# Kernel tuning notes

Hardware: AMD Instinct MI355X
Metric: run time of the kernel (lower is better)

The kernel has to match this reference:

```python
import jax, jax.numpy as jnp
import numpy as np

VOCAB = 32000
HIDDEN = 512
B, T = 8, 512
LN_EPS = 1e-5


def setup_inputs() -> dict:
    key = jax.random.key(0)
    ks = jax.random.split(key, 9)
    s = 0.02
    return {
        "input_ids": jax.random.randint(ks[0], (B, T), 0, VOCAB),
        "emb": jax.random.normal(ks[1], (VOCAB, HIDDEN), jnp.float32) * s,
        "w_ih": jax.random.normal(ks[2], (3 * HIDDEN, HIDDEN), jnp.float32) * s,
        "w_hh": jax.random.normal(ks[3], (3 * HIDDEN, HIDDEN), jnp.float32) * s,
        "b_ih": jnp.zeros((3 * HIDDEN,), jnp.float32),
        "b_hh": jnp.zeros((3 * HIDDEN,), jnp.float32),
        "ln_gamma": jnp.ones((HIDDEN,), jnp.float32),
        "ln_beta": jnp.zeros((HIDDEN,), jnp.float32),
        "head_w": jax.random.normal(ks[4], (VOCAB, HIDDEN), jnp.float32) * s,
        "head_b": jnp.zeros((VOCAB,), jnp.float32),
    }


def _gru_scan(xg, w_hh, b_hh):
    # xg: [T, B, 3H]  (input-side gate pre-activations, PyTorch gate order r,z,n)
    H = xg.shape[-1] // 3
    h0 = jnp.zeros((xg.shape[1], H), xg.dtype)

    def step(h, xg_t):
        hg = h @ w_hh.T + b_hh              # [B, 3H]
        xr, xz, xn = jnp.split(xg_t, 3, axis=-1)
        hr, hz, hn = jnp.split(hg, 3, axis=-1)
        r = jax.nn.sigmoid(xr + hr)
        z = jax.nn.sigmoid(xz + hz)
        n = jnp.tanh(xn + r * hn)
        h_new = (1.0 - z) * n + z * h
        return h_new, h_new

    _, hs = jax.lax.scan(step, h0, xg)
    return hs  # [T, B, H]


def reference(input_ids, emb, w_ih, w_hh, b_ih, b_hh, ln_gamma, ln_beta, head_w, head_b):
    # embedding lookup: [B, T, H]
    x = emb[input_ids]
    # precompute input-side gate pre-activations for all timesteps: [B, T, 3H]
    xg = jnp.einsum("bth,gh->btg", x, w_ih) + b_ih
    # sequential GRU over time
    hs = _gru_scan(jnp.swapaxes(xg, 0, 1), w_hh, b_hh)  # [T, B, H]
    hs = jnp.swapaxes(hs, 0, 1)                          # [B, T, H]
    # LayerNorm over hidden dim
    mu = jnp.mean(hs, axis=-1, keepdims=True)
    var = jnp.mean(jnp.square(hs - mu), axis=-1, keepdims=True)
    y = (hs - mu) * jax.lax.rsqrt(var + LN_EPS) * ln_gamma + ln_beta
    # output head: [B, T, V]
    logits = jnp.einsum("bth,vh->btv", y, head_w) + head_b
    return logits
```

## Files before the change

### kernel.cpp

```cpp
#include <hip/hip_runtime.h>
#include <hip/hip_bf16.h>
#include <stdint.h>

#define VOCAB 32000
#define HID 512
#define NB 8
#define SEQ 512
#define NG 1536
#define LN_EPS 1e-5f
#define GRU_WGS 32
#define GRU_SPIN_BUDGET (1 << 20)

typedef short bf16x8 __attribute__((ext_vector_type(8)));
typedef float f32x4 __attribute__((ext_vector_type(4)));

__device__ __forceinline__ unsigned short f2bf(float f) {
  union { float f; uint32_t u; } c; c.f = f;
  return (unsigned short)((c.u + 0x7fffu + ((c.u >> 16) & 1u)) >> 16);
}

__global__ void init_ws_kernel(unsigned short* h_state, int* flags) {
  int i = blockIdx.x * 256 + threadIdx.x;
  if (i < 2 * 16 * HID) h_state[i] = 0;
  if (i < GRU_WGS * 16) flags[i] = 0;
}

__global__ void conv_bf16_kernel(const float* __restrict__ in,
                                 unsigned short* __restrict__ out, int n4) {
  int i = blockIdx.x * 256 + threadIdx.x;
  if (i >= n4) return;
  const float4 v = ((const float4*)in)[i];
  ushort4 o;
  o.x = f2bf(v.x); o.y = f2bf(v.y); o.z = f2bf(v.z); o.w = f2bf(v.w);
  ((ushort4*)out)[i] = o;
}

__global__ void embed_kernel(const int* __restrict__ ids,
                             const float* __restrict__ emb,
                             unsigned short* __restrict__ out) {
  int row = blockIdx.x;
  int id = ids[row];
  int c = threadIdx.x * 2;
  const float2 v = *(const float2*)(emb + (size_t)id * HID + c);
  ushort2 o; o.x = f2bf(v.x); o.y = f2bf(v.y);
  *(ushort2*)(out + (size_t)row * HID + c) = o;
}

#define BM 128
#define BN 128
#define BK 32

__global__ __launch_bounds__(256, 2) void gemm_bt_kernel(
    const unsigned short* __restrict__ A, const unsigned short* __restrict__ B,
    const float* __restrict__ bias, float* __restrict__ C, int N, int nbn) {
  __shared__ unsigned short a_lds[BM * BK];
  __shared__ unsigned short b_lds[BN * BK];
  const int nwg = gridDim.x;
  const int chunk = nwg >> 3;
  const int bid = blockIdx.x;
  const int sw = (bid & 7) * chunk + (bid >> 3);
  const int bm = sw / nbn, bn = sw % nbn;
  const int tid = threadIdx.x;
  const int lane = tid & 63, wid = tid >> 6;
  const int wm = wid >> 1, wn = wid & 1;

  f32x4 acc[4][4] = {};

  for (int kt = 0; kt < HID / BK; ++kt) {
    __syncthreads();
#pragma unroll
    for (int p = 0; p < 2; ++p) {
      const int flat = (p * 256 + tid) * 16;
      const int row = flat >> 6;
      const int kb = flat & 63;
      const char* ga =
          (const char*)(A + ((size_t)(bm * BM + row) * HID + kt * BK)) + kb;
      const char* gb =
          (const char*)(B + ((size_t)(bn * BN + row) * HID + kt * BK)) + kb;
      char* la = (char*)a_lds + (size_t)(p * 256 + wid * 64) * 16;
      char* lb = (char*)b_lds + (size_t)(p * 256 + wid * 64) * 16;
      __builtin_amdgcn_global_load_lds(
          (const __attribute__((address_space(1))) void*)ga,
          (__attribute__((address_space(3))) void*)la, 16, 0, 0);
      __builtin_amdgcn_global_load_lds(
          (const __attribute__((address_space(1))) void*)gb,
          (__attribute__((address_space(3))) void*)lb, 16, 0, 0);
    }
    __syncthreads();
    bf16x8 af[4], bfr[4];
#pragma unroll
    for (int i = 0; i < 4; ++i) {
      af[i] = *(const bf16x8*)(a_lds + (wm * 64 + i * 16 + (lane & 15)) * BK +
                               (lane >> 4) * 8);
      bfr[i] = *(const bf16x8*)(b_lds + (wn * 64 + i * 16 + (lane & 15)) * BK +
                                (lane >> 4) * 8);
    }
#pragma unroll
    for (int i = 0; i < 4; ++i)
#pragma unroll
      for (int j = 0; j < 4; ++j)
        acc[i][j] =
            __builtin_amdgcn_mfma_f32_16x16x32_bf16(af[i], bfr[j], acc[i][j], 0, 0, 0);
  }
#pragma unroll
  for (int i = 0; i < 4; ++i) {
    const int mrow = bm * BM + wm * 64 + i * 16 + (lane >> 4) * 4;
#pragma unroll
    for (int j = 0; j < 4; ++j) {
      const int col = bn * BN + wn * 64 + j * 16 + (lane & 15);
      const float bv = bias[col];
#pragma unroll
      for (int r = 0; r < 4; ++r)
        C[(size_t)(mrow + r) * N + col] = acc[i][j][r] + bv;
    }
  }
}

__global__ __launch_bounds__(64, 1) void gru_kernel(
    const float* __restrict__ xg, const float* __restrict__ w_hh,
    const float* __restrict__ b_hh, float* __restrict__ hs,
    unsigned short* h_state, int* flags) {
  const int wid = blockIdx.x;
  const int lane = threadIdx.x;
  const int col16 = lane & 15;
  const int kq = lane >> 4;

  __shared__ float h_pub[8][16];

  bf16x8 wf[3][16];
#pragma unroll
  for (int g = 0; g < 3; ++g) {
    const float* wr =
        w_hh + (size_t)(g * HID + wid * 16 + col16) * HID + kq * 8;
#pragma unroll
    for (int kk = 0; kk < 16; ++kk) {
      float4 f0 = *(const float4*)(wr + kk * 32);
      float4 f1 = *(const float4*)(wr + kk * 32 + 4);
      bf16x8 v;
      v[0] = (short)f2bf(f0.x); v[1] = (short)f2bf(f0.y);
      v[2] = (short)f2bf(f0.z); v[3] = (short)f2bf(f0.w);
      v[4] = (short)f2bf(f1.x); v[5] = (short)f2bf(f1.y);
      v[6] = (short)f2bf(f1.z); v[7] = (short)f2bf(f1.w);
      wf[g][kk] = v;
    }
  }
  const float bh_r = b_hh[0 * HID + wid * 16 + col16];
  const float bh_z = b_hh[1 * HID + wid * 16 + col16];
  const float bh_n = b_hh[2 * HID + wid * 16 + col16];

  const int abase = col16 * HID + kq * 8;
  const bool realrow = col16 < 8;
  const bool owner = lane < 32;
  const int bbase = kq * 4;

  float xr[4], xz[4], xn[4];
#pragma unroll
  for (int r = 0; r < 4; ++r) { xr[r] = 0.f; xz[r] = 0.f; xn[r] = 0.f; }
  if (owner) {
#pragma unroll
    for (int r = 0; r < 4; ++r) {
      const size_t xo = (size_t)(bbase + r) * SEQ * NG + wid * 16 + col16;
      xr[r] = xg[xo];
      xz[r] = xg[xo + HID];
      xn[r] = xg[xo + 2 * HID];
    }
  }
  float hprev[4] = {0.f, 0.f, 0.f, 0.f};
  int budget = GRU_SPIN_BUDGET;

  for (int t = 0; t < SEQ; ++t) {
    while (budget > 0) {
      int v = t;
      if (lane < 32)
        v = __hip_atomic_load(flags + lane * 16, __ATOMIC_RELAXED,
                              __HIP_MEMORY_SCOPE_AGENT);
      if (__ballot(v >= t) == ~0ULL) break;
      --budget;
      __builtin_amdgcn_s_sleep(1);
    }

    const unsigned short* rd = h_state + (size_t)(t & 1) * (16 * HID);
    unsigned short* wpub = h_state + (size_t)((t + 1) & 1) * (16 * HID);

    uint64_t hb[32];
#pragma unroll
    for (int kk = 0; kk < 32; ++kk) hb[kk] = 0;
    if (realrow) {
#pragma unroll
      for (int kk = 0; kk < 16; ++kk) {
        const uint64_t* ap = (const uint64_t*)(rd + abase + kk * 32);
        hb[2 * kk] =
            __hip_atomic_load(ap, __ATOMIC_RELAXED, __HIP_MEMORY_SCOPE_AGENT);
        hb[2 * kk + 1] = __hip_atomic_load(ap + 1, __ATOMIC_RELAXED,
                                           __HIP_MEMORY_SCOPE_AGENT);
      }
    }

    f32x4 ar = {0.f, 0.f, 0.f, 0.f};
    f32x4 az = {0.f, 0.f, 0.f, 0.f};
    f32x4 an = {0.f, 0.f, 0.f, 0.f};
#pragma unroll
    for (int kk = 0; kk < 16; ++kk) {
      union { uint64_t u[2]; bf16x8 v; } cv;
      cv.u[0] = hb[2 * kk]; cv.u[1] = hb[2 * kk + 1];
      ar = __builtin_amdgcn_mfma_f32_16x16x32_bf16(cv.v, wf[0][kk], ar, 0, 0, 0);
      az = __builtin_amdgcn_mfma_f32_16x16x32_bf16(cv.v, wf[1][kk], az, 0, 0, 0);
      an = __builtin_amdgcn_mfma_f32_16x16x32_bf16(cv.v, wf[2][kk], an, 0, 0, 0);
    }

    float hnew[4];
    if (owner) {
#pragma unroll
      for (int r = 0; r < 4; ++r) {
        const float rg = 1.f / (1.f + __expf(-(xr[r] + ar[r] + bh_r)));
        const float zg = 1.f / (1.f + __expf(-(xz[r] + az[r] + bh_z)));
        const float a = xn[r] + rg * (an[r] + bh_n);
        const float e2 = __expf(-2.f * fabsf(a));
        const float nn = copysignf((1.f - e2) / (1.f + e2), a);
        hnew[r] = (1.f - zg) * nn + zg * hprev[r];
        hprev[r] = hnew[r];
        h_pub[bbase + r][col16] = hnew[r];
      }
    }
    asm volatile("" ::: "memory");
    {
      const int tb = lane >> 3;
      const int tc = (lane & 7) * 2;
      const float2 hp = *(const float2*)&h_pub[tb][tc];
      union { unsigned short s[2]; uint32_t u; } pk;
      pk.s[0] = f2bf(hp.x);
      pk.s[1] = f2bf(hp.y);
      uint32_t* dst = (uint32_t*)(wpub + tb * HID + wid * 16 + tc);
      __hip_atomic_store(dst, pk.u, __ATOMIC_RELAXED,
                         __HIP_MEMORY_SCOPE_AGENT);
    }
    asm volatile("s_waitcnt vmcnt(0)" ::: "memory");
    if (lane == 0)
      __hip_atomic_store(flags + wid * 16, t + 1, __ATOMIC_RELAXED,
                         __HIP_MEMORY_SCOPE_AGENT);
    if (owner) {
#pragma unroll
      for (int r = 0; r < 4; ++r)
        hs[((size_t)(bbase + r) * SEQ + t) * HID + wid * 16 + col16] = hnew[r];
      if (t + 1 < SEQ) {
#pragma unroll
        for (int r = 0; r < 4; ++r) {
          const size_t xo = (size_t)(bbase + r) * SEQ * NG +
                            (size_t)(t + 1) * NG + wid * 16 + col16;
          xr[r] = xg[xo];
          xz[r] = xg[xo + HID];
          xn[r] = xg[xo + 2 * HID];
        }
      }
    }
  }
}

__global__ __launch_bounds__(256) void ln_kernel(
    const float* __restrict__ hs, const float* __restrict__ gamma,
    const float* __restrict__ beta, unsigned short* __restrict__ y) {
  const int row = blockIdx.x * 4 + (threadIdx.x >> 6);
  const int lane = threadIdx.x & 63;
  const float* x = hs + (size_t)row * HID + lane * 8;
  float v[8];
  *(float4*)v = *(const float4*)x;
  *(float4*)(v + 4) = *(const float4*)(x + 4);
  float s = 0.f, q = 0.f;
#pragma unroll
  for (int j = 0; j < 8; ++j) { s += v[j]; q += v[j] * v[j]; }
#pragma unroll
  for (int off = 32; off > 0; off >>= 1) {
    s += __shfl_xor(s, off);
    q += __shfl_xor(q, off);
  }
  const float mu = s * (1.f / 512.f);
  const float is = rsqrtf(q * (1.f / 512.f) - mu * mu + LN_EPS);
  const float* gp = gamma + lane * 8;
  const float* bp = beta + lane * 8;
  union { unsigned short o[8]; uint4 u; } pk;
#pragma unroll
  for (int j = 0; j < 8; ++j) pk.o[j] = f2bf((v[j] - mu) * is * gp[j] + bp[j]);
  *(uint4*)(y + (size_t)row * HID + lane * 8) = pk.u;
}

extern "C" void kernel_launch(void* const* d_in, const int* in_sizes, int n_in,
                              void* d_out, int out_size, void* d_ws,
                              size_t ws_size, hipStream_t stream) {
  const int* ids = (const int*)d_in[0];
  const float* emb = (const float*)d_in[1];
  const float* w_ih = (const float*)d_in[2];
  const float* w_hh = (const float*)d_in[3];
  const float* b_ih = (const float*)d_in[4];
  const float* b_hh = (const float*)d_in[5];
  const float* gamma = (const float*)d_in[6];
  const float* beta = (const float*)d_in[7];
  const float* head_w = (const float*)d_in[8];
  const float* head_b = (const float*)d_in[9];
  float* out = (float*)d_out;

  char* ws = (char*)d_ws;
  size_t off = 0;
  auto alloc = [&](size_t bytes) -> void* {
    void* p = ws + off;
    off = (off + bytes + 255) & ~(size_t)255;
    return p;
  };
  int* flags = (int*)alloc(GRU_WGS * 16 * sizeof(int));
  unsigned short* h_state = (unsigned short*)alloc(2 * 16 * HID * 2);
  unsigned short* A1 = (unsigned short*)alloc((size_t)NB * SEQ * HID * 2);
  unsigned short* wihb = (unsigned short*)alloc((size_t)NG * HID * 2);
  unsigned short* hwb = (unsigned short*)alloc((size_t)VOCAB * HID * 2);
  float* xg = (float*)alloc((size_t)NB * SEQ * NG * 4);
  float* hsb = (float*)alloc((size_t)NB * SEQ * HID * 4);
  unsigned short* yb = (unsigned short*)alloc((size_t)NB * SEQ * HID * 2);

  init_ws_kernel<<<64, 256, 0, stream>>>(h_state, flags);
  conv_bf16_kernel<<<(NG * HID / 4) / 256, 256, 0, stream>>>(w_ih, wihb,
                                                             NG * HID / 4);
  conv_bf16_kernel<<<(VOCAB * HID / 4) / 256, 256, 0, stream>>>(
      head_w, hwb, VOCAB * HID / 4);
  embed_kernel<<<NB * SEQ, 256, 0, stream>>>(ids, emb, A1);
  gemm_bt_kernel<<<(NB * SEQ / BM) * (NG / BN), 256, 0, stream>>>(
      A1, wihb, b_ih, xg, NG, NG / BN);
  gru_kernel<<<GRU_WGS, 64, 0, stream>>>(xg, w_hh, b_hh, hsb, h_state, flags);
  ln_kernel<<<NB * SEQ / 4, 256, 0, stream>>>(hsb, gamma, beta, yb);
  gemm_bt_kernel<<<(NB * SEQ / BM) * (VOCAB / BN), 256, 0, stream>>>(
      yb, hwb, head_b, out, VOCAB, VOCAB / BN);
}
```

Measured before the change: 1.724 ms.

## Embed step parity in bf16 LSBs to replace GRU flag barrier

Drops the per-workgroup flag array and its spin barrier in the persistent GRU kernel. Each published bf16 hidden value now carries a step-parity tag in its low mantissa bit, and readers poll the hidden-state buffer itself until every tag matches the expected parity. This removes one round trip per step (store h, wait for vmcnt, store flag, poll flags, then load h). The change also prefetches the next step's xg before the MFMAs, splits each accumulator into two chains for more instruction-level parallelism, and publishes with 64-bit stores. It costs one bit of bf16 precision on half the elements, and correctness depends on each 64-bit store becoming visible atomically.

New measurement: 1.778 ms. +3.1%, slower.

```diff
diff --git a/kernel.cpp b/kernel.cpp
--- a/kernel.cpp
+++ b/kernel.cpp
@@ -19,10 +19,10 @@
   return (unsigned short)((c.u + 0x7fffu + ((c.u >> 16) & 1u)) >> 16);
 }
 
-__global__ void init_ws_kernel(unsigned short* h_state, int* flags) {
+__global__ void init_ws_kernel(uint32_t* h_state) {
   int i = blockIdx.x * 256 + threadIdx.x;
-  if (i < 2 * 16 * HID) h_state[i] = 0;
-  if (i < GRU_WGS * 16) flags[i] = 0;
+  if (i < 8 * HID) h_state[i] = 0u;
+  else if (i < 16 * HID) h_state[i] = 0x00010001u;
 }
 
 __global__ void conv_bf16_kernel(const float* __restrict__ in,
@@ -119,7 +119,7 @@
 __global__ __launch_bounds__(64, 1) void gru_kernel(
     const float* __restrict__ xg, const float* __restrict__ w_hh,
     const float* __restrict__ b_hh, float* __restrict__ hs,
-    unsigned short* h_state, int* flags) {
+    unsigned short* h_state) {
   const int wid = blockIdx.x;
   const int lane = threadIdx.x;
   const int col16 = lane & 15;
@@ -169,46 +169,71 @@
   int budget = GRU_SPIN_BUDGET;
 
   for (int t = 0; t < SEQ; ++t) {
-    while (budget > 0) {
-      int v = t;
-      if (lane < 32)
-        v = __hip_atomic_load(flags + lane * 16, __ATOMIC_RELAXED,
-                              __HIP_MEMORY_SCOPE_AGENT);
-      if (__ballot(v >= t) == ~0ULL) break;
-      --budget;
-      __builtin_amdgcn_s_sleep(1);
-    }
-
     const unsigned short* rd = h_state + (size_t)(t & 1) * (16 * HID);
     unsigned short* wpub = h_state + (size_t)((t + 1) & 1) * (16 * HID);
+    const uint32_t texp = (uint32_t)((t >> 1) & 1);
+    const uint32_t tpub = (uint32_t)(((t + 1) >> 1) & 1);
 
     uint64_t hb[32];
 #pragma unroll
     for (int kk = 0; kk < 32; ++kk) hb[kk] = 0;
-    if (realrow) {
-#pragma unroll
-      for (int kk = 0; kk < 16; ++kk) {
-        const uint64_t* ap = (const uint64_t*)(rd + abase + kk * 32);
-        hb[2 * kk] =
-            __hip_atomic_load(ap, __ATOMIC_RELAXED, __HIP_MEMORY_SCOPE_AGENT);
-        hb[2 * kk + 1] = __hip_atomic_load(ap + 1, __ATOMIC_RELAXED,
+    {
+      bool ok = false;
+      while (!ok && budget > 0) {
+        uint32_t bad = 0;
+        if (realrow) {
+#pragma unroll
+          for (int kk = 0; kk < 16; ++kk) {
+            const uint64_t* ap = (const uint64_t*)(rd + abase + kk * 32);
+            hb[2 * kk] = __hip_atomic_load(ap, __ATOMIC_RELAXED,
                                            __HIP_MEMORY_SCOPE_AGENT);
+            hb[2 * kk + 1] = __hip_atomic_load(ap + 1, __ATOMIC_RELAXED,
+                                               __HIP_MEMORY_SCOPE_AGENT);
+          }
+#pragma unroll
+          for (int kk = 0; kk < 32; ++kk) {
+            bad |= (uint32_t)hb[kk] ^ texp;
+            bad |= (uint32_t)(hb[kk] >> 32) ^ texp;
+          }
+          bad &= 1u;
+        }
+        ok = (__ballot(bad == 0u) == ~0ULL);
+        --budget;
       }
     }
 
-    f32x4 ar = {0.f, 0.f, 0.f, 0.f};
-    f32x4 az = {0.f, 0.f, 0.f, 0.f};
-    f32x4 an = {0.f, 0.f, 0.f, 0.f};
-#pragma unroll
-    for (int kk = 0; kk < 16; ++kk) {
-      union { uint64_t u[2]; bf16x8 v; } cv;
-      cv.u[0] = hb[2 * kk]; cv.u[1] = hb[2 * kk + 1];
-      ar = __builtin_amdgcn_mfma_f32_16x16x32_bf16(cv.v, wf[0][kk], ar, 0, 0, 0);
-      az = __builtin_amdgcn_mfma_f32_16x16x32_bf16(cv.v, wf[1][kk], az, 0, 0, 0);
-      an = __builtin_amdgcn_mfma_f32_16x16x32_bf16(cv.v, wf[2][kk], an, 0, 0, 0);
-    }
-
-    float hnew[4];
+    float xrn[4], xzn[4], xnn[4];
+#pragma unroll
+    for (int r = 0; r < 4; ++r) { xrn[r] = 0.f; xzn[r] = 0.f; xnn[r] = 0.f; }
+    if (owner && t + 1 < SEQ) {
+#pragma unroll
+      for (int r = 0; r < 4; ++r) {
+        const size_t xo = (size_t)(bbase + r) * SEQ * NG +
+                          (size_t)(t + 1) * NG + wid * 16 + col16;
+        xrn[r] = xg[xo];
+        xzn[r] = xg[xo + HID];
+        xnn[r] = xg[xo + 2 * HID];
+      }
+    }
+
+    f32x4 ar0 = {0.f, 0.f, 0.f, 0.f}, ar1 = {0.f, 0.f, 0.f, 0.f};
+    f32x4 az0 = {0.f, 0.f, 0.f, 0.f}, az1 = {0.f, 0.f, 0.f, 0.f};
+    f32x4 an0 = {0.f, 0.f, 0.f, 0.f}, an1 = {0.f, 0.f, 0.f, 0.f};
+#pragma unroll
+    for (int kk = 0; kk < 16; kk += 2) {
+      union { uint64_t u[2]; bf16x8 v; } c0, c1;
+      c0.u[0] = hb[2 * kk];     c0.u[1] = hb[2 * kk + 1];
+      c1.u[0] = hb[2 * kk + 2]; c1.u[1] = hb[2 * kk + 3];
+      ar0 = __builtin_amdgcn_mfma_f32_16x16x32_bf16(c0.v, wf[0][kk], ar0, 0, 0, 0);
+      az0 = __builtin_amdgcn_mfma_f32_16x16x32_bf16(c0.v, wf[1][kk], az0, 0, 0, 0);
+      an0 = __builtin_amdgcn_mfma_f32_16x16x32_bf16(c0.v, wf[2][kk], an0, 0, 0, 0);
+      ar1 = __builtin_amdgcn_mfma_f32_16x16x32_bf16(c1.v, wf[0][kk + 1], ar1, 0, 0, 0);
+      az1 = __builtin_amdgcn_mfma_f32_16x16x32_bf16(c1.v, wf[1][kk + 1], az1, 0, 0, 0);
+      an1 = __builtin_amdgcn_mfma_f32_16x16x32_bf16(c1.v, wf[2][kk + 1], an1, 0, 0, 0);
+    }
+    const f32x4 ar = ar0 + ar1, az = az0 + az1, an = an0 + an1;
+
+    float hnew[4] = {0.f, 0.f, 0.f, 0.f};
     if (owner) {
 #pragma unroll
       for (int r = 0; r < 4; ++r) {
@@ -222,37 +247,28 @@
         h_pub[bbase + r][col16] = hnew[r];
       }
     }
-    asm volatile("" ::: "memory");
-    {
-      const int tb = lane >> 3;
-      const int tc = (lane & 7) * 2;
-      const float2 hp = *(const float2*)&h_pub[tb][tc];
-      union { unsigned short s[2]; uint32_t u; } pk;
-      pk.s[0] = f2bf(hp.x);
+    asm volatile("s_waitcnt lgkmcnt(0)" ::: "memory");
+    __builtin_amdgcn_sched_barrier(0);
+    if (lane < 32) {
+      const int tb = lane >> 2;
+      const int tq = (lane & 3) * 4;
+      const float4 hp = *(const float4*)&h_pub[tb][tq];
+      union { unsigned short s[4]; uint64_t u; } pk;
+      pk.s[0] = (unsigned short)((f2bf(hp.x) & ~(unsigned short)1) | tpub);
       pk.s[1] = f2bf(hp.y);
-      uint32_t* dst = (uint32_t*)(wpub + tb * HID + wid * 16 + tc);
+      pk.s[2] = (unsigned short)((f2bf(hp.z) & ~(unsigned short)1) | tpub);
+      pk.s[3] = f2bf(hp.w);
+      uint64_t* dst = (uint64_t*)(wpub + tb * HID + wid * 16 + tq);
       __hip_atomic_store(dst, pk.u, __ATOMIC_RELAXED,
                          __HIP_MEMORY_SCOPE_AGENT);
     }
-    asm volatile("s_waitcnt vmcnt(0)" ::: "memory");
-    if (lane == 0)
-      __hip_atomic_store(flags + wid * 16, t + 1, __ATOMIC_RELAXED,
-                         __HIP_MEMORY_SCOPE_AGENT);
     if (owner) {
 #pragma unroll
       for (int r = 0; r < 4; ++r)
         hs[((size_t)(bbase + r) * SEQ + t) * HID + wid * 16 + col16] = hnew[r];
-      if (t + 1 < SEQ) {
-#pragma unroll
-        for (int r = 0; r < 4; ++r) {
-          const size_t xo = (size_t)(bbase + r) * SEQ * NG +
-                            (size_t)(t + 1) * NG + wid * 16 + col16;
-          xr[r] = xg[xo];
-          xz[r] = xg[xo + HID];
-          xn[r] = xg[xo + 2 * HID];
-        }
-      }
-    }
+    }
+#pragma unroll
+    for (int r = 0; r < 4; ++r) { xr[r] = xrn[r]; xz[r] = xzn[r]; xn[r] = xnn[r]; }
   }
 }
 
@@ -305,7 +321,6 @@
     off = (off + bytes + 255) & ~(size_t)255;
     return p;
   };
-  int* flags = (int*)alloc(GRU_WGS * 16 * sizeof(int));
   unsigned short* h_state = (unsigned short*)alloc(2 * 16 * HID * 2);
   unsigned short* A1 = (unsigned short*)alloc((size_t)NB * SEQ * HID * 2);
   unsigned short* wihb = (unsigned short*)alloc((size_t)NG * HID * 2);
@@ -314,7 +329,7 @@
   float* hsb = (float*)alloc((size_t)NB * SEQ * HID * 4);
   unsigned short* yb = (unsigned short*)alloc((size_t)NB * SEQ * HID * 2);
 
-  init_ws_kernel<<<64, 256, 0, stream>>>(h_state, flags);
+  init_ws_kernel<<<32, 256, 0, stream>>>((uint32_t*)h_state);
   conv_bf16_kernel<<<(NG * HID / 4) / 256, 256, 0, stream>>>(w_ih, wihb,
                                                              NG * HID / 4);
   conv_bf16_kernel<<<(VOCAB * HID / 4) / 256, 256, 0, stream>>>(
@@ -322,7 +337,7 @@
   embed_kernel<<<NB * SEQ, 256, 0, stream>>>(ids, emb, A1);
   gemm_bt_kernel<<<(NB * SEQ / BM) * (NG / BN), 256, 0, stream>>>(
       A1, wihb, b_ih, xg, NG, NG / BN);
-  gru_kernel<<<GRU_WGS, 64, 0, stream>>>(xg, w_hh, b_hh, hsb, h_state, flags);
+  gru_kernel<<<GRU_WGS, 64, 0, stream>>>(xg, w_hh, b_hh, hsb, h_state);
   ln_kernel<<<NB * SEQ / 4, 256, 0, stream>>>(hsb, gamma, beta, yb);
   gemm_bt_kernel<<<(NB * SEQ / BM) * (VOCAB / BN), 256, 0, stream>>>(
       yb, hwb, head_b, out, VOCAB, VOCAB / BN);
```

## Fuse GRU, LayerNorm and head GEMM into one persistent kernel with overlap

Applied to the files above, without the earlier changes.

Replaces the separate GRU, LayerNorm and head GEMM launches with a single persistent kernel. 32 workgroups run the GRU recurrence while 224 worker workgroups spin on per-timestep flags and compute LayerNorm plus the output projection for 16-timestep tiles as soon as those hidden states exist. LayerNorm is folded into the A-operand staging of the GEMM, which removes the bf16 y buffer. The aim is to hide the long serial GRU behind the large vocab GEMM. The cost is a GEMM loop that is less pipelined (no double buffering, A loaded through atomics), plus a dependence on all 256 workgroups being co-resident, with spin budgets as a fallback.

New measurement: 1.957 ms. 13.5% more time.

```diff
diff --git a/kernel.cpp b/kernel.cpp
--- a/kernel.cpp
+++ b/kernel.cpp
@@ -9,7 +9,12 @@
 #define NG 1536
 #define LN_EPS 1e-5f
 #define GRU_WGS 32
+#define NWORK 224
+#define TW 16
+#define NTW (SEQ / TW)
+#define NBN (VOCAB / 128)
 #define GRU_SPIN_BUDGET (1 << 20)
+#define WRK_SPIN_BUDGET (1 << 22)
 
 typedef short bf16x8 __attribute__((ext_vector_type(8)));
 typedef float f32x4 __attribute__((ext_vector_type(4)));
@@ -116,171 +121,276 @@
   }
 }
 
-__global__ __launch_bounds__(64, 1) void gru_kernel(
+__global__ __launch_bounds__(256, 1) void mega_kernel(
     const float* __restrict__ xg, const float* __restrict__ w_hh,
     const float* __restrict__ b_hh, float* __restrict__ hs,
-    unsigned short* h_state, int* flags) {
-  const int wid = blockIdx.x;
-  const int lane = threadIdx.x;
-  const int col16 = lane & 15;
-  const int kq = lane >> 4;
-
+    unsigned short* __restrict__ h_state, int* __restrict__ flags,
+    const unsigned short* __restrict__ hwb, const float* __restrict__ head_b,
+    const float* __restrict__ gamma, const float* __restrict__ beta,
+    float* __restrict__ out) {
   __shared__ float h_pub[8][16];
-
-  bf16x8 wf[3][16];
-#pragma unroll
-  for (int g = 0; g < 3; ++g) {
-    const float* wr =
-        w_hh + (size_t)(g * HID + wid * 16 + col16) * HID + kq * 8;
-#pragma unroll
-    for (int kk = 0; kk < 16; ++kk) {
-      float4 f0 = *(const float4*)(wr + kk * 32);
-      float4 f1 = *(const float4*)(wr + kk * 32 + 4);
-      bf16x8 v;
-      v[0] = (short)f2bf(f0.x); v[1] = (short)f2bf(f0.y);
-      v[2] = (short)f2bf(f0.z); v[3] = (short)f2bf(f0.w);
-      v[4] = (short)f2bf(f1.x); v[5] = (short)f2bf(f1.y);
-      v[6] = (short)f2bf(f1.z); v[7] = (short)f2bf(f1.w);
-      wf[g][kk] = v;
-    }
-  }
-  const float bh_r = b_hh[0 * HID + wid * 16 + col16];
-  const float bh_z = b_hh[1 * HID + wid * 16 + col16];
-  const float bh_n = b_hh[2 * HID + wid * 16 + col16];
-
-  const int abase = col16 * HID + kq * 8;
-  const bool realrow = col16 < 8;
-  const bool owner = lane < 32;
-  const int bbase = kq * 4;
-
-  float xr[4], xz[4], xn[4];
-#pragma unroll
-  for (int r = 0; r < 4; ++r) { xr[r] = 0.f; xz[r] = 0.f; xn[r] = 0.f; }
-  if (owner) {
-#pragma unroll
-    for (int r = 0; r < 4; ++r) {
-      const size_t xo = (size_t)(bbase + r) * SEQ * NG + wid * 16 + col16;
-      xr[r] = xg[xo];
-      xz[r] = xg[xo + HID];
-      xn[r] = xg[xo + 2 * HID];
-    }
-  }
-  float hprev[4] = {0.f, 0.f, 0.f, 0.f};
-  int budget = GRU_SPIN_BUDGET;
-
-  for (int t = 0; t < SEQ; ++t) {
-    while (budget > 0) {
-      int v = t;
-      if (lane < 32)
-        v = __hip_atomic_load(flags + lane * 16, __ATOMIC_RELAXED,
-                              __HIP_MEMORY_SCOPE_AGENT);
-      if (__ballot(v >= t) == ~0ULL) break;
-      --budget;
-      __builtin_amdgcn_s_sleep(1);
-    }
-
-    const unsigned short* rd = h_state + (size_t)(t & 1) * (16 * HID);
-    unsigned short* wpub = h_state + (size_t)((t + 1) & 1) * (16 * HID);
-
-    uint64_t hb[32];
-#pragma unroll
-    for (int kk = 0; kk < 32; ++kk) hb[kk] = 0;
-    if (realrow) {
+  __shared__ unsigned short a_lds[128 * 32];
+  __shared__ unsigned short b_lds[128 * 32];
+  __shared__ float mu_lds[128];
+  __shared__ float is_lds[128];
+
+  const int tid = threadIdx.x;
+
+  if (blockIdx.x < GRU_WGS) {
+    if (tid >= 64) return;
+    const int wid = blockIdx.x;
+    const int lane = tid;
+    const int col16 = lane & 15;
+    const int kq = lane >> 4;
+
+    bf16x8 wf[3][16];
+#pragma unroll
+    for (int g = 0; g < 3; ++g) {
+      const float* wr =
+          w_hh + (size_t)(g * HID + wid * 16 + col16) * HID + kq * 8;
 #pragma unroll
       for (int kk = 0; kk < 16; ++kk) {
-        const uint64_t* ap = (const uint64_t*)(rd + abase + kk * 32);
-        hb[2 * kk] =
-            __hip_atomic_load(ap, __ATOMIC_RELAXED, __HIP_MEMORY_SCOPE_AGENT);
-        hb[2 * kk + 1] = __hip_atomic_load(ap + 1, __ATOMIC_RELAXED,
-                                           __HIP_MEMORY_SCOPE_AGENT);
-      }
-    }
-
-    f32x4 ar = {0.f, 0.f, 0.f, 0.f};
-    f32x4 az = {0.f, 0.f, 0.f, 0.f};
-    f32x4 an = {0.f, 0.f, 0.f, 0.f};
-#pragma unroll
-    for (int kk = 0; kk < 16; ++kk) {
-      union { uint64_t u[2]; bf16x8 v; } cv;
-      cv.u[0] = hb[2 * kk]; cv.u[1] = hb[2 * kk + 1];
-      ar = __builtin_amdgcn_mfma_f32_16x16x32_bf16(cv.v, wf[0][kk], ar, 0, 0, 0);
-      az = __builtin_amdgcn_mfma_f32_16x16x32_bf16(cv.v, wf[1][kk], az, 0, 0, 0);
-      an = __builtin_amdgcn_mfma_f32_16x16x32_bf16(cv.v, wf[2][kk], an, 0, 0, 0);
-    }
-
-    float hnew[4];
+        float4 f0 = *(const float4*)(wr + kk * 32);
+        float4 f1 = *(const float4*)(wr + kk * 32 + 4);
+        bf16x8 v;
+        v[0] = (short)f2bf(f0.x); v[1] = (short)f2bf(f0.y);
+        v[2] = (short)f2bf(f0.z); v[3] = (short)f2bf(f0.w);
+        v[4] = (short)f2bf(f1.x); v[5] = (short)f2bf(f1.y);
+        v[6] = (short)f2bf(f1.z); v[7] = (short)f2bf(f1.w);
+        wf[g][kk] = v;
+      }
+    }
+    const float bh_r = b_hh[0 * HID + wid * 16 + col16];
+    const float bh_z = b_hh[1 * HID + wid * 16 + col16];
+    const float bh_n = b_hh[2 * HID + wid * 16 + col16];
+
+    const int abase = col16 * HID + kq * 8;
+    const bool realrow = col16 < 8;
+    const bool owner = lane < 32;
+    const int bbase = kq * 4;
+
+    float xr[4], xz[4], xn[4];
+#pragma unroll
+    for (int r = 0; r < 4; ++r) { xr[r] = 0.f; xz[r] = 0.f; xn[r] = 0.f; }
     if (owner) {
 #pragma unroll
       for (int r = 0; r < 4; ++r) {
-        const float rg = 1.f / (1.f + __expf(-(xr[r] + ar[r] + bh_r)));
-        const float zg = 1.f / (1.f + __expf(-(xz[r] + az[r] + bh_z)));
-        const float a = xn[r] + rg * (an[r] + bh_n);
-        const float e2 = __expf(-2.f * fabsf(a));
-        const float nn = copysignf((1.f - e2) / (1.f + e2), a);
-        hnew[r] = (1.f - zg) * nn + zg * hprev[r];
-        hprev[r] = hnew[r];
-        h_pub[bbase + r][col16] = hnew[r];
-      }
-    }
-    asm volatile("" ::: "memory");
-    {
-      const int tb = lane >> 3;
-      const int tc = (lane & 7) * 2;
-      const float2 hp = *(const float2*)&h_pub[tb][tc];
-      union { unsigned short s[2]; uint32_t u; } pk;
-      pk.s[0] = f2bf(hp.x);
-      pk.s[1] = f2bf(hp.y);
-      uint32_t* dst = (uint32_t*)(wpub + tb * HID + wid * 16 + tc);
-      __hip_atomic_store(dst, pk.u, __ATOMIC_RELAXED,
-                         __HIP_MEMORY_SCOPE_AGENT);
-    }
-    asm volatile("s_waitcnt vmcnt(0)" ::: "memory");
-    if (lane == 0)
-      __hip_atomic_store(flags + wid * 16, t + 1, __ATOMIC_RELAXED,
-                         __HIP_MEMORY_SCOPE_AGENT);
-    if (owner) {
-#pragma unroll
-      for (int r = 0; r < 4; ++r)
-        hs[((size_t)(bbase + r) * SEQ + t) * HID + wid * 16 + col16] = hnew[r];
-      if (t + 1 < SEQ) {
+        const size_t xo = (size_t)(bbase + r) * SEQ * NG + wid * 16 + col16;
+        xr[r] = xg[xo];
+        xz[r] = xg[xo + HID];
+        xn[r] = xg[xo + 2 * HID];
+      }
+    }
+    float hprev[4] = {0.f, 0.f, 0.f, 0.f};
+    int budget = GRU_SPIN_BUDGET;
+
+    for (int t = 0; t < SEQ; ++t) {
+      while (budget > 0) {
+        int v = t;
+        if (lane < 32)
+          v = __hip_atomic_load(flags + lane * 16, __ATOMIC_RELAXED,
+                                __HIP_MEMORY_SCOPE_AGENT);
+        if (__ballot(v >= t) == ~0ULL) break;
+        --budget;
+        __builtin_amdgcn_s_sleep(1);
+      }
+
+      const unsigned short* rd = h_state + (size_t)(t & 1) * (16 * HID);
+      unsigned short* wpub = h_state + (size_t)((t + 1) & 1) * (16 * HID);
+
+      uint64_t hb[32];
+#pragma unroll
+      for (int kk = 0; kk < 32; ++kk) hb[kk] = 0;
+      if (realrow) {
+#pragma unroll
+        for (int kk = 0; kk < 16; ++kk) {
+          const uint64_t* ap = (const uint64_t*)(rd + abase + kk * 32);
+          hb[2 * kk] = __hip_atomic_load(ap, __ATOMIC_RELAXED,
+                                         __HIP_MEMORY_SCOPE_AGENT);
+          hb[2 * kk + 1] = __hip_atomic_load(ap + 1, __ATOMIC_RELAXED,
+                                             __HIP_MEMORY_SCOPE_AGENT);
+        }
+      }
+
+      f32x4 ar = {0.f, 0.f, 0.f, 0.f};
+      f32x4 az = {0.f, 0.f, 0.f, 0.f};
+      f32x4 an = {0.f, 0.f, 0.f, 0.f};
+#pragma unroll
+      for (int kk = 0; kk < 16; ++kk) {
+        union { uint64_t u[2]; bf16x8 v; } cv;
+        cv.u[0] = hb[2 * kk]; cv.u[1] = hb[2 * kk + 1];
+        ar = __builtin_amdgcn_mfma_f32_16x16x32_bf16(cv.v, wf[0][kk], ar, 0, 0, 0);
+        az = __builtin_amdgcn_mfma_f32_16x16x32_bf16(cv.v, wf[1][kk], az, 0, 0, 0);
+        an = __builtin_amdgcn_mfma_f32_16x16x32_bf16(cv.v, wf[2][kk], an, 0, 0, 0);
+      }
+
+      if (owner) {
+#pragma unroll
+        for (int r = 0; r < 4; ++r) {
+          const float rg = 1.f / (1.f + __expf(-(xr[r] + ar[r] + bh_r)));
+          const float zg = 1.f / (1.f + __expf(-(xz[r] + az[r] + bh_z)));
+          const float a = xn[r] + rg * (an[r] + bh_n);
+          const float e2 = __expf(-2.f * fabsf(a));
+          const float nn = copysignf((1.f - e2) / (1.f + e2), a);
+          const float hnew = (1.f - zg) * nn + zg * hprev[r];
+          hprev[r] = hnew;
+          h_pub[bbase + r][col16] = hnew;
+          union { float f; uint32_t u; } cv; cv.f = hnew;
+          uint32_t* hp = (uint32_t*)(hs + ((size_t)(bbase + r) * SEQ + t) * HID +
+                                     wid * 16 + col16);
+          __hip_atomic_store(hp, cv.u, __ATOMIC_RELAXED,
+                             __HIP_MEMORY_SCOPE_AGENT);
+        }
+      }
+      asm volatile("s_waitcnt lgkmcnt(0)" ::: "memory");
+      __builtin_amdgcn_sched_barrier(0);
+      {
+        const int tb = lane >> 3;
+        const int tc = (lane & 7) * 2;
+        const float2 hp = *(const float2*)&h_pub[tb][tc];
+        union { unsigned short s[2]; uint32_t u; } pk;
+        pk.s[0] = f2bf(hp.x);
+        pk.s[1] = f2bf(hp.y);
+        uint32_t* dst = (uint32_t*)(wpub + tb * HID + wid * 16 + tc);
+        __hip_atomic_store(dst, pk.u, __ATOMIC_RELAXED,
+                           __HIP_MEMORY_SCOPE_AGENT);
+      }
+      asm volatile("s_waitcnt vmcnt(0)" ::: "memory");
+      if (lane == 0)
+        __hip_atomic_store(flags + wid * 16, t + 1, __ATOMIC_RELAXED,
+                           __HIP_MEMORY_SCOPE_AGENT);
+      if (owner && t + 1 < SEQ) {
 #pragma unroll
         for (int r = 0; r < 4; ++r) {
           const size_t xo = (size_t)(bbase + r) * SEQ * NG +
                             (size_t)(t + 1) * NG + wid * 16 + col16;
-          xr[r] = xg[xo];
-          xz[r] = xg[xo + HID];
-          xn[r] = xg[xo + 2 * HID];
+          xr[r] = xg[xo]; xz[r] = xg[xo + HID]; xn[r] = xg[xo + 2 * HID];
         }
       }
     }
+    return;
   }
-}
-
-__global__ __launch_bounds__(256) void ln_kernel(
-    const float* __restrict__ hs, const float* __restrict__ gamma,
-    const float* __restrict__ beta, unsigned short* __restrict__ y) {
-  const int row = blockIdx.x * 4 + (threadIdx.x >> 6);
-  const int lane = threadIdx.x & 63;
-  const float* x = hs + (size_t)row * HID + lane * 8;
-  float v[8];
-  *(float4*)v = *(const float4*)x;
-  *(float4*)(v + 4) = *(const float4*)(x + 4);
-  float s = 0.f, q = 0.f;
-#pragma unroll
-  for (int j = 0; j < 8; ++j) { s += v[j]; q += v[j] * v[j]; }
-#pragma unroll
-  for (int off = 32; off > 0; off >>= 1) {
-    s += __shfl_xor(s, off);
-    q += __shfl_xor(q, off);
+
+  const int w = blockIdx.x - GRU_WGS;
+  const int lane = tid & 63, wv = tid >> 6;
+  const int wm = wv >> 1, wn = wv & 1;
+
+  for (int ti = w; ti < NTW * NBN; ti += NWORK) {
+    const int twi = ti / NBN;
+    const int bn = ti - twi * NBN;
+    const int t0 = twi * TW;
+    const int tneed = t0 + TW;
+
+    if (tid < 64) {
+      int bud = WRK_SPIN_BUDGET;
+      while (bud-- > 0) {
+        int v = 0x7fffffff;
+        if (lane < 32)
+          v = __hip_atomic_load(flags + lane * 16, __ATOMIC_RELAXED,
+                                __HIP_MEMORY_SCOPE_AGENT);
+        if (__ballot(v >= tneed) == ~0ULL) break;
+        __builtin_amdgcn_s_sleep(8);
+      }
+    }
+    __syncthreads();
+
+    for (int rr = 0; rr < 32; ++rr) {
+      const int i = wv * 32 + rr;
+      const int grow = ((i >> 4) * SEQ) + t0 + (i & 15);
+      const uint64_t* xp = (const uint64_t*)(hs + (size_t)grow * HID) + lane * 4;
+      float s = 0.f, q = 0.f;
+#pragma unroll
+      for (int j = 0; j < 4; ++j) {
+        union { uint64_t u; float f[2]; } cv;
+        cv.u = __hip_atomic_load(xp + j, __ATOMIC_RELAXED,
+                                 __HIP_MEMORY_SCOPE_AGENT);
+        s += cv.f[0] + cv.f[1];
+        q += cv.f[0] * cv.f[0] + cv.f[1] * cv.f[1];
+      }
+#pragma unroll
+      for (int off = 32; off > 0; off >>= 1) {
+        s += __shfl_xor(s, off);
+        q += __shfl_xor(q, off);
+      }
+      if (lane == 0) {
+        const float mu = s * (1.f / 512.f);
+        mu_lds[i] = mu;
+        is_lds[i] = rsqrtf(q * (1.f / 512.f) - mu * mu + LN_EPS);
+      }
+    }
+    __syncthreads();
+
+    f32x4 acc[4][4] = {};
+    for (int kt = 0; kt < 16; ++kt) {
+      __syncthreads();
+#pragma unroll
+      for (int p = 0; p < 2; ++p) {
+        const int flat = (p * 256 + tid) * 16;
+        const int row = flat >> 6;
+        const int kb = flat & 63;
+        const char* gb =
+            (const char*)(hwb + ((size_t)(bn * 128 + row) * HID + kt * 32)) + kb;
+        char* lb = (char*)b_lds + (size_t)(p * 256 + wv * 64) * 16;
+        __builtin_amdgcn_global_load_lds(
+            (const __attribute__((address_space(1))) void*)gb,
+            (__attribute__((address_space(3))) void*)lb, 16, 0, 0);
+      }
+      {
+        const int arow = tid >> 1, ah = (tid & 1) * 16;
+        const int grow = ((arow >> 4) * SEQ) + t0 + (arow & 15);
+        const uint64_t* ap =
+            (const uint64_t*)(hs + (size_t)grow * HID + kt * 32 + ah);
+        float av[16];
+#pragma unroll
+        for (int j = 0; j < 8; ++j) {
+          union { uint64_t u; float f[2]; } cv;
+          cv.u = __hip_atomic_load(ap + j, __ATOMIC_RELAXED,
+                                   __HIP_MEMORY_SCOPE_AGENT);
+          av[2 * j] = cv.f[0];
+          av[2 * j + 1] = cv.f[1];
+        }
+        const float mu = mu_lds[arow], isv = is_lds[arow];
+        const float* gp = gamma + kt * 32 + ah;
+        const float* bp = beta + kt * 32 + ah;
+        union { unsigned short s[16]; uint4 u[2]; } pk;
+#pragma unroll
+        for (int j = 0; j < 16; ++j)
+          pk.s[j] = f2bf((av[j] - mu) * isv * gp[j] + bp[j]);
+        uint4* ad = (uint4*)((char*)a_lds + arow * 64 + ah * 2);
+        ad[0] = pk.u[0];
+        ad[1] = pk.u[1];
+      }
+      __syncthreads();
+      bf16x8 af[4], bfr[4];
+#pragma unroll
+      for (int i = 0; i < 4; ++i) {
+        af[i] = *(const bf16x8*)(a_lds + (wm * 64 + i * 16 + (lane & 15)) * 32 +
+                                 (lane >> 4) * 8);
+        bfr[i] = *(const bf16x8*)(b_lds + (wn * 64 + i * 16 + (lane & 15)) * 32 +
+                                  (lane >> 4) * 8);
+      }
+#pragma unroll
+      for (int i = 0; i < 4; ++i)
+#pragma unroll
+        for (int j = 0; j < 4; ++j)
+          acc[i][j] = __builtin_amdgcn_mfma_f32_16x16x32_bf16(af[i], bfr[j],
+                                                              acc[i][j], 0, 0, 0);
+    }
+#pragma unroll
+    for (int i = 0; i < 4; ++i) {
+#pragma unroll
+      for (int j = 0; j < 4; ++j) {
+        const int col = bn * 128 + wn * 64 + j * 16 + (lane & 15);
+        const float bv = head_b[col];
+#pragma unroll
+        for (int r = 0; r < 4; ++r) {
+          const int mrowl = wm * 64 + i * 16 + (lane >> 4) * 4 + r;
+          const int grow = ((mrowl >> 4) * SEQ) + t0 + (mrowl & 15);
+          out[(size_t)grow * VOCAB + col] = acc[i][j][r] + bv;
+        }
+      }
+    }
   }
-  const float mu = s * (1.f / 512.f);
-  const float is = rsqrtf(q * (1.f / 512.f) - mu * mu + LN_EPS);
-  const float* gp = gamma + lane * 8;
-  const float* bp = beta + lane * 8;
-  union { unsigned short o[8]; uint4 u; } pk;
-#pragma unroll
-  for (int j = 0; j < 8; ++j) pk.o[j] = f2bf((v[j] - mu) * is * gp[j] + bp[j]);
-  *(uint4*)(y + (size_t)row * HID + lane * 8) = pk.u;
 }
 
 extern "C" void kernel_launch(void* const* d_in, const int* in_sizes, int n_in,
@@ -312,7 +422,6 @@
   unsigned short* hwb = (unsigned short*)alloc((size_t)VOCAB * HID * 2);
   float* xg = (float*)alloc((size_t)NB * SEQ * NG * 4);
   float* hsb = (float*)alloc((size_t)NB * SEQ * HID * 4);
-  unsigned short* yb = (unsigned short*)alloc((size_t)NB * SEQ * HID * 2);
 
   init_ws_kernel<<<64, 256, 0, stream>>>(h_state, flags);
   conv_bf16_kernel<<<(NG * HID / 4) / 256, 256, 0, stream>>>(w_ih, wihb,
@@ -322,8 +431,6 @@
   embed_kernel<<<NB * SEQ, 256, 0, stream>>>(ids, emb, A1);
   gemm_bt_kernel<<<(NB * SEQ / BM) * (NG / BN), 256, 0, stream>>>(
       A1, wihb, b_ih, xg, NG, NG / BN);
-  gru_kernel<<<GRU_WGS, 64, 0, stream>>>(xg, w_hh, b_hh, hsb, h_state, flags);
-  ln_kernel<<<NB * SEQ / 4, 256, 0, stream>>>(hsb, gamma, beta, yb);
-  gemm_bt_kernel<<<(NB * SEQ / BM) * (VOCAB / BN), 256, 0, stream>>>(
-      yb, hwb, head_b, out, VOCAB, VOCAB / BN);
-}
+  mega_kernel<<<GRU_WGS + NWORK, 256, 0, stream>>>(
+      xg, w_hh, b_hh, hsb, h_state, flags, hwb, head_b, gamma, beta, out);
+}
```
